# Optimization experiments

Hardware: AMD Instinct MI355X
Metric: run time of the kernel (lower is better)

Reference implementation:

```python
import jax, jax.numpy as jnp
import numpy as np

BN_EPS = 1e-5


def setup_inputs() -> dict:
    key = jax.random.key(0)
    ks = jax.random.split(key, 9)
    N, C, T, V, S, INTER, OUT = 64, 64, 300, 25, 3, 16, 64
    return {
        "x": jax.random.normal(ks[0], (N, C, T, V), dtype=jnp.float32),
        "A": jax.random.uniform(ks[1], (S, V, V), dtype=jnp.float32),
        "PA": jax.random.normal(ks[2], (S, V, V), dtype=jnp.float32) * 1e-3,
        "Wa": jax.random.normal(ks[3], (S, INTER, C), dtype=jnp.float32) * 0.1,
        "ba": jax.random.normal(ks[4], (S, INTER), dtype=jnp.float32) * 0.1,
        "Wb": jax.random.normal(ks[5], (S, INTER, C), dtype=jnp.float32) * 0.1,
        "bb": jax.random.normal(ks[6], (S, INTER), dtype=jnp.float32) * 0.1,
        "Wd": jax.random.normal(ks[7], (S, OUT, C), dtype=jnp.float32) * 0.1,
        "bd": jax.random.normal(ks[8], (S, OUT), dtype=jnp.float32) * 0.1,
        "gamma": jnp.ones((OUT,), dtype=jnp.float32),
        "beta": jnp.zeros((OUT,), dtype=jnp.float32),
    }


def reference(x, A, PA, Wa, ba, Wb, bb, Wd, bd, gamma, beta):
    N, C, T, V = x.shape
    S, INTER = Wa.shape[0], Wa.shape[1]
    K = INTER * T  # contraction length for attention

    # 1x1 convs for all subsets at once: [N,S,inter,T,V]
    fa = jnp.einsum('nctv,sic->nsitv', x, Wa) + ba[None, :, :, None, None]
    fb = jnp.einsum('nctv,sic->nsitv', x, Wb) + bb[None, :, :, None, None]

    # A1: permute(0,3,1,2).view(N,V,inter*T)  -> [N,S,V,K]
    A1 = fa.transpose(0, 1, 4, 2, 3).reshape(N, S, V, K)
    # A2: view(N,inter*T,V)                   -> [N,S,K,V]
    A2 = fb.reshape(N, S, K, V)

    # attention: softmax over dim=-2, plus learned adjacency
    att = jnp.einsum('nsvk,nskw->nsvw', A1, A2) / jnp.asarray(K, x.dtype)
    att = jax.nn.softmax(att, axis=-2) + (A + PA)[None]  # [N,S,V,V]

    # message passing: x.view(N,C*T,V) @ att, then 1x1 conv_d, summed over subsets
    xm = jnp.einsum('nkv,nsvw->nskw', x.reshape(N, C * T, V), att)
    xm = xm.reshape(N, S, C, T, V)
    y = jnp.einsum('nsctv,soc->notv', xm, Wd) + bd.sum(0)[None, :, None, None]

    # BatchNorm2d (training-mode batch stats, per-channel over N,T,V)
    mean = y.mean(axis=(0, 2, 3), keepdims=True)
    var = y.var(axis=(0, 2, 3), keepdims=True)
    y = gamma[None, :, None, None] * (y - mean) * jax.lax.rsqrt(var + BN_EPS) \
        + beta[None, :, None, None]

    # residual (in_channels == out_channels -> identity down) + relu
    return jax.nn.relu(y + x)
```

## Files before the change

### kernel.cpp

```cpp
#include <hip/hip_runtime.h>
#include <math.h>

constexpr int Nn = 64, Cc = 64, Tt = 300, Vv = 25, Ss = 3, Ii = 16, Oo = 64;
constexpr int TVc  = Tt * Vv;
constexpr int CTVc = Cc * TVc;
constexpr float KINV = 1.0f / 4800.0f;

constexpr int WS_ATT  = 0;
constexpr int WS_SUM  = 120000;
constexpr int WS_SQ   = 120512;
constexpr int WS_MEAN = 121024;
constexpr int WS_RSTD = 121088;
constexpr int WS_ZERO_FLOATS = 121024;
constexpr int WS_XB_F   = 121152;
constexpr int WS_WAB_F  = WS_XB_F + 15360000;
constexpr int WS_WDB_F  = WS_WAB_F + 3072;
constexpr int WS_ATTB_F = WS_WDB_F + 6144;
constexpr int WS_END_F  = WS_ATTB_F + 98304;
constexpr size_t WS_NEED = (size_t)WS_END_F * 4;

typedef __attribute__((ext_vector_type(8))) short bf16x8;
typedef __attribute__((ext_vector_type(4))) short short4v;
typedef __attribute__((ext_vector_type(4))) float f32x4;
typedef __attribute__((ext_vector_type(16))) float f32x16;
typedef __attribute__((ext_vector_type(4))) int int4v;

__device__ __forceinline__ short f2bf(float f) {
    unsigned u = __builtin_bit_cast(unsigned, f);
    u += 0x7FFFu + ((u >> 16) & 1u);
    return (short)(u >> 16);
}
__device__ __forceinline__ float bf2f(short s) {
    unsigned u = ((unsigned)(unsigned short)s) << 16;
    return __builtin_bit_cast(float, u);
}
__device__ __forceinline__ void store4(float* p, f32x4 v) {
    __builtin_memcpy(p, &v, 16);
}

__global__ __launch_bounds__(256) void k0_xpose(
    const float* __restrict__ x, short* __restrict__ xb)
{
    const int n   = blockIdx.y;
    const int tid = threadIdx.x;
    const int tv  = blockIdx.x * 32 + (tid & 31);
    const int g   = (tid >> 5) & 7;
    if (tv >= TVc) return;
    const float* xp = x + (size_t)n * CTVc + (size_t)(g * 8) * TVc + tv;
    bf16x8 o;
    #pragma unroll
    for (int j = 0; j < 8; ++j) o[j] = f2bf(xp[(size_t)j * TVc]);
    *(bf16x8*)(xb + ((size_t)n * TVc + tv) * 64 + g * 8) = o;
}

__global__ __launch_bounds__(256) void kpack(
    const float* __restrict__ Wa, const float* __restrict__ Wb,
    const float* __restrict__ Wd, short* __restrict__ wab, short* __restrict__ wdb)
{
    const int i = blockIdx.x * 256 + threadIdx.x;
    if (i < 6144) {
        const int s = i >> 11, rb = i & 2047, r = rb >> 6, c = rb & 63;
        const float v = (r < 16) ? Wa[(s * 16 + r) * 64 + c]
                                 : Wb[(s * 16 + (r - 16)) * 64 + c];
        wab[i] = f2bf(v);
    }
    if (i < 12288) wdb[i] = f2bf(Wd[i]);
}

template<bool XB>
__device__ __forceinline__ void load_xfrag(
    const float* __restrict__ xn, const short* __restrict__ xbn,
    int tv, bool ok, int quad, bf16x8& b0, bf16x8& b1)
{
    if constexpr (XB) {
        const short* bp = xbn + (ok ? tv : 0) * 64 + quad * 8;
        b0 = *(const bf16x8*)bp;
        b1 = *(const bf16x8*)(bp + 32);
    } else {
        const float* bp = xn + (quad * 8) * TVc + tv;
        #pragma unroll
        for (int j = 0; j < 8; ++j) {
            b0[j] = f2bf(ok ? bp[j * TVc] : 0.0f);
            b1[j] = f2bf(ok ? bp[(j + 32) * TVc] : 0.0f);
        }
    }
}

template<bool XB>
__global__ __launch_bounds__(256) void ka_gram_mfma(
    const float* __restrict__ x, const short* __restrict__ xb,
    const short* __restrict__ wab,
    const float* __restrict__ Wa, const float* __restrict__ ba,
    const float* __restrict__ Wb, const float* __restrict__ bb,
    float* __restrict__ att)
{
    __shared__ short uT[112 * 104];
    __shared__ float part[4 * 1024];
    __shared__ float bab[96];

    const int tid = threadIdx.x;
    const int t0  = blockIdx.x * 4;
    const int n   = blockIdx.y;
    const float* xn  = x + n * CTVc + t0 * 25;
    const short* xbn = XB ? (xb + ((size_t)n * TVc + t0 * 25) * 64) : nullptr;

    if (tid < 96) {
        const int s = tid >> 5, r = tid & 31;
        bab[tid] = (r < 16) ? ba[s * 16 + r] : bb[s * 16 + r - 16];
    }

    const int lane = tid & 63;
    const int wave = tid >> 6;
    const int l16  = lane & 15;
    const int quad = lane >> 4;

    bf16x8 afr[3][2][2];
    #pragma unroll
    for (int s = 0; s < 3; ++s)
        #pragma unroll
        for (int half = 0; half < 2; ++half)
            #pragma unroll
            for (int k = 0; k < 2; ++k) {
                if constexpr (XB) {
                    afr[s][half][k] = *(const bf16x8*)(
                        wab + (s * 32 + half * 16 + l16) * 64 + k * 32 + quad * 8);
                } else {
                    const float* W = half ? Wb : Wa;
                    const float* wp = W + (s * 16 + l16) * 64 + k * 32 + quad * 8;
                    const float4 w0 = *(const float4*)wp;
                    const float4 w1 = *(const float4*)(wp + 4);
                    bf16x8 a;
                    a[0] = f2bf(w0.x); a[1] = f2bf(w0.y); a[2] = f2bf(w0.z); a[3] = f2bf(w0.w);
                    a[4] = f2bf(w1.x); a[5] = f2bf(w1.y); a[6] = f2bf(w1.z); a[7] = f2bf(w1.w);
                    afr[s][half][k] = a;
                }
            }
    __syncthreads();

    for (int nt = wave; nt < 7; nt += 4) {
        const int tv = nt * 16 + l16;
        const bool ok = tv < 100;
        bf16x8 b0, b1;
        load_xfrag<XB>(xn, xbn, tv, ok, quad, b0, b1);
        #pragma unroll
        for (int s = 0; s < 3; ++s)
            #pragma unroll
            for (int half = 0; half < 2; ++half) {
                f32x4 acc = {0.0f, 0.0f, 0.0f, 0.0f};
                acc = __builtin_amdgcn_mfma_f32_16x16x32_bf16(afr[s][half][0], b0, acc, 0, 0, 0);
                acc = __builtin_amdgcn_mfma_f32_16x16x32_bf16(afr[s][half][1], b1, acc, 0, 0, 0);
                const float4 bv = *(const float4*)(bab + s * 32 + half * 16 + quad * 4);
                short4v pk;
                pk[0] = f2bf(acc[0] + bv.x); pk[1] = f2bf(acc[1] + bv.y);
                pk[2] = f2bf(acc[2] + bv.z); pk[3] = f2bf(acc[3] + bv.w);
                *(short4v*)(uT + tv * 104 + s * 32 + half * 16 + quad * 4) = pk;
            }
    }
    __syncthreads();

    const int t   = wave;
    const int w32 = lane & 31;
    const int khi = lane >> 5;
    f32x16 g[3];
    #pragma unroll
    for (int s = 0; s < 3; ++s)
        #pragma unroll
        for (int r = 0; r < 16; ++r) g[s][r] = 0.0f;

    #pragma unroll
    for (int s = 0; s < 3; ++s) {
        const short* base = uT + (t * 25 + w32) * 104 + s * 32 + khi * 8;
        const bf16x8 aA = *(const bf16x8*)(base);
        const bf16x8 bB = *(const bf16x8*)(base + 16);
        g[s] = __builtin_amdgcn_mfma_f32_32x32x16_bf16(aA, bB, g[s], 0, 0, 0);
    }

    for (int s = 0; s < 3; ++s) {
        __syncthreads();
        #pragma unroll
        for (int r = 0; r < 16; ++r) {
            const int row = (r & 3) + 8 * (r >> 2) + 4 * khi;
            part[wave * 1024 + row * 32 + w32] = g[s][r];
        }
        __syncthreads();
        float* attns = att + (n * 3 + s) * 625;
        for (int p = tid; p < 625; p += 256) {
            const int v = p / 25, w = p - v * 25;
            const int q = v * 32 + w;
            atomicAdd(attns + p, part[q] + part[1024 + q] + part[2048 + q] + part[3072 + q]);
        }
    }
}

template<bool ATTB>
__global__ __launch_bounds__(64) void kb_softmax(
    float* __restrict__ att, const float* __restrict__ A, const float* __restrict__ PA,
    short* __restrict__ attb)
{
    const int b = blockIdx.x;
    const int s = b % 3;
    const int w = threadIdx.x;
    if (w >= 32) return;
    float col[25] = {};
    if (w < 25) {
        float* base = att + b * 625;
        float m = -1e30f;
        #pragma unroll
        for (int v = 0; v < 25; ++v) {
            col[v] = base[v * 25 + w] * KINV;
            m = fmaxf(m, col[v]);
        }
        float sum = 0.0f;
        #pragma unroll
        for (int v = 0; v < 25; ++v) { col[v] = expf(col[v] - m); sum += col[v]; }
        const float inv = 1.0f / sum;
        #pragma unroll
        for (int v = 0; v < 25; ++v) {
            col[v] = fmaf(col[v], inv, A[(s * 25 + v) * 25 + w] + PA[(s * 25 + v) * 25 + w]);
            base[v * 25 + w] = col[v];
        }
    }
    if constexpr (ATTB) {
        short* dst = attb + b * 1024 + w * 32;
        #pragma unroll
        for (int v = 0; v < 25; ++v) dst[v] = (w < 25) ? f2bf(col[v]) : (short)0;
        #pragma unroll
        for (int v = 25; v < 32; ++v) dst[v] = 0;
    }
}

__global__ __launch_bounds__(512, 4) void k3_y_mfma(
    const short* __restrict__ xb, const short* __restrict__ wdb,
    const short* __restrict__ attb, float* __restrict__ y, float* __restrict__ bns)
{
    __shared__ __align__(16) short U[192 * 128];
    __shared__ float bnA[8][32], bnB[8][32];

    const int tid = threadIdx.x;
    const int t0  = blockIdx.x * 4;
    const int n   = blockIdx.y;
    const short* xbn = xb + ((size_t)n * TVc + t0 * 25) * 64;

    const int lane = tid & 63;
    const int wave = tid >> 6;
    const int l16  = lane & 15;
    const int quad = lane >> 4;

    for (int i = tid; i < 3072; i += 512)
        ((int4v*)U)[i] = (int4v){0, 0, 0, 0};
    __syncthreads();

    if (wave < 7) {
        const int tv = wave * 16 + l16;
        const bool ok = tv < 100;
        const short* bp = xbn + (ok ? tv : 0) * 64 + quad * 8;
        const bf16x8 b0 = *(const bf16x8*)bp;
        const bf16x8 b1 = *(const bf16x8*)(bp + 32);
        const int tl  = tv / 25;
        const int vp  = tv - tl * 25;
        const int col = tl * 32 + vp;
        const int grp = col >> 3, ing = col & 7;
        #pragma unroll
        for (int s = 0; s < 3; ++s)
            #pragma unroll
            for (int m = 0; m < 4; ++m) {
                const short* wp = wdb + (s * 64 + m * 16 + l16) * 64 + quad * 8;
                const bf16x8 f0 = *(const bf16x8*)wp;
                const bf16x8 f1 = *(const bf16x8*)(wp + 32);
                f32x4 acc = {0.0f, 0.0f, 0.0f, 0.0f};
                acc = __builtin_amdgcn_mfma_f32_16x16x32_bf16(f0, b0, acc, 0, 0, 0);
                acc = __builtin_amdgcn_mfma_f32_16x16x32_bf16(f1, b1, acc, 0, 0, 0);
                if (ok) {
                    #pragma unroll
                    for (int r = 0; r < 4; ++r) {
                        const int row = s * 64 + m * 16 + quad * 4 + r;
                        U[row * 128 + (((grp ^ (row & 15)) << 3) | ing)] = f2bf(acc[r]);
                    }
                }
            }
    }
    __syncthreads();

    const int t  = wave >> 1;
    const int ob = (wave & 1) * 32;
    f32x4 D[2][2];
    #pragma unroll
    for (int mt = 0; mt < 2; ++mt)
        #pragma unroll
        for (int nb = 0; nb < 2; ++nb) D[mt][nb] = (f32x4){0.0f, 0.0f, 0.0f, 0.0f};
    #pragma unroll
    for (int s = 0; s < 3; ++s) {
        const short* ab = attb + (size_t)(n * 3 + s) * 1024 + l16 * 32 + quad * 8;
        const bf16x8 a0 = *(const bf16x8*)ab;
        const bf16x8 a1 = *(const bf16x8*)(ab + 512);
        #pragma unroll
        for (int nb = 0; nb < 2; ++nb) {
            const int row = s * 64 + ob + nb * 16 + l16;
            const bf16x8 bv = *(const bf16x8*)(
                U + row * 128 + (((t * 4 + quad) ^ (row & 15)) << 3));
            D[0][nb] = __builtin_amdgcn_mfma_f32_16x16x32_bf16(a0, bv, D[0][nb], 0, 0, 0);
            D[1][nb] = __builtin_amdgcn_mfma_f32_16x16x32_bf16(a1, bv, D[1][nb], 0, 0, 0);
        }
    }

    float s1[2] = {0.0f, 0.0f}, s2[2] = {0.0f, 0.0f};
    #pragma unroll
    for (int nb = 0; nb < 2; ++nb) {
        const int og = ob + nb * 16 + l16;
        float* dst = y + ((size_t)(n * 64 + og) * 300 + t0 + t) * 25;
        const f32x4 d0 = D[0][nb];
        store4(dst + quad * 4, d0);
        s1[nb] += d0[0] + d0[1] + d0[2] + d0[3];
        s2[nb] += d0[0]*d0[0] + d0[1]*d0[1] + d0[2]*d0[2] + d0[3]*d0[3];
        const f32x4 d1 = D[1][nb];
        if (quad < 2) {
            store4(dst + 16 + quad * 4, d1);
            s1[nb] += d1[0] + d1[1] + d1[2] + d1[3];
            s2[nb] += d1[0]*d1[0] + d1[1]*d1[1] + d1[2]*d1[2] + d1[3]*d1[3];
        } else if (quad == 2) {
            dst[24] = d1[0];
            s1[nb] += d1[0];
            s2[nb] += d1[0] * d1[0];
        }
    }
    #pragma unroll
    for (int nb = 0; nb < 2; ++nb) {
        s1[nb] += __shfl_xor(s1[nb], 16); s1[nb] += __shfl_xor(s1[nb], 32);
        s2[nb] += __shfl_xor(s2[nb], 16); s2[nb] += __shfl_xor(s2[nb], 32);
    }
    if (lane < 16) {
        bnA[wave][lane]      = s1[0];
        bnA[wave][16 + lane] = s1[1];
        bnB[wave][lane]      = s2[0];
        bnB[wave][16 + lane] = s2[1];
    }
    __syncthreads();
    if (tid < 64) {
        const int o = tid, h = o >> 5, i = o & 31;
        const float S1 = bnA[h][i] + bnA[h + 2][i] + bnA[h + 4][i] + bnA[h + 6][i];
        const float S2 = bnB[h][i] + bnB[h + 2][i] + bnB[h + 4][i] + bnB[h + 6][i];
        const int cp = (blockIdx.x & 7) * 64;
        atomicAdd(bns + cp + o, S1);
        atomicAdd(bns + 512 + cp + o, S2);
    }
}

__global__ __launch_bounds__(256) void k3_y_mfma_fb(
    const float* __restrict__ x, const float* __restrict__ Wd,
    const float* __restrict__ att, float* __restrict__ y, float* __restrict__ bns)
{
    __shared__ __align__(16) short U[96 * 128];
    __shared__ __align__(16) short attT[3 * 1024];
    __shared__ float bn1[4][32], bn2[4][32];

    const int tid = threadIdx.x;
    const int t0  = blockIdx.x * 4;
    const int n   = blockIdx.y;
    const int oh  = blockIdx.z;
    const float* xn = x + n * CTVc + t0 * 25;

    const int lane = tid & 63;
    const int wave = tid >> 6;
    const int l16  = lane & 15;
    const int quad = lane >> 4;

    for (int i = tid; i < 1536; i += 256)
        ((int4v*)U)[i] = (int4v){0, 0, 0, 0};
    for (int i = tid; i < 3072; i += 256) {
        const int s = i >> 10, r = i & 1023, v = r >> 5, vp = r & 31;
        const float val = (v < 25 && vp < 25) ? att[(n * 3 + s) * 625 + vp * 25 + v] : 0.0f;
        attT[i] = f2bf(val);
    }
    bf16x8 afr[3][2][2];
    #pragma unroll
    for (int s = 0; s < 3; ++s)
        #pragma unroll
        for (int m = 0; m < 2; ++m)
            #pragma unroll
            for (int k = 0; k < 2; ++k) {
                const float* wp = Wd + ((s * 64 + oh * 32 + m * 16 + l16) * 64) + k * 32 + quad * 8;
                const float4 w0 = *(const float4*)wp;
                const float4 w1 = *(const float4*)(wp + 4);
                bf16x8 a;
                a[0] = f2bf(w0.x); a[1] = f2bf(w0.y); a[2] = f2bf(w0.z); a[3] = f2bf(w0.w);
                a[4] = f2bf(w1.x); a[5] = f2bf(w1.y); a[6] = f2bf(w1.z); a[7] = f2bf(w1.w);
                afr[s][m][k] = a;
            }
    __syncthreads();

    for (int nt = wave; nt < 7; nt += 4) {
        const int tv = nt * 16 + l16;
        const bool ok = tv < 100;
        bf16x8 b0, b1;
        load_xfrag<false>(xn, nullptr, tv, ok, quad, b0, b1);
        const int tl  = tv / 25;
        const int vp  = tv - tl * 25;
        const int col = tl * 32 + vp;
        const int grp = col >> 3, ing = col & 7;
        #pragma unroll
        for (int s = 0; s < 3; ++s)
            #pragma unroll
            for (int m = 0; m < 2; ++m) {
                f32x4 acc = {0.0f, 0.0f, 0.0f, 0.0f};
                acc = __builtin_amdgcn_mfma_f32_16x16x32_bf16(afr[s][m][0], b0, acc, 0, 0, 0);
                acc = __builtin_amdgcn_mfma_f32_16x16x32_bf16(afr[s][m][1], b1, acc, 0, 0, 0);
                if (ok) {
                    #pragma unroll
                    for (int r = 0; r < 4; ++r) {
                        const int row = s * 32 + m * 16 + quad * 4 + r;
                        U[row * 128 + (((grp ^ (row & 15)) << 3) | ing)] = f2bf(acc[r]);
                    }
                }
            }
    }
    __syncthreads();

    const int t = wave;
    bf16x8 aF[3][2], bF[3][2];
    #pragma unroll
    for (int s = 0; s < 3; ++s) {
        #pragma unroll
        for (int mt = 0; mt < 2; ++mt)
            aF[s][mt] = *(const bf16x8*)(attT + s * 1024 + (mt * 16 + l16) * 32 + quad * 8);
        #pragma unroll
        for (int nb = 0; nb < 2; ++nb) {
            const int row = s * 32 + nb * 16 + l16;
            bF[s][nb] = *(const bf16x8*)(U + row * 128 + (((t * 4 + quad) ^ (row & 15)) << 3));
        }
    }
    f32x4 D[2][2];
    #pragma unroll
    for (int mt = 0; mt < 2; ++mt)
        #pragma unroll
        for (int nb = 0; nb < 2; ++nb) D[mt][nb] = (f32x4){0.0f, 0.0f, 0.0f, 0.0f};
    #pragma unroll
    for (int s = 0; s < 3; ++s)
        #pragma unroll
        for (int mt = 0; mt < 2; ++mt)
            #pragma unroll
            for (int nb = 0; nb < 2; ++nb)
                D[mt][nb] = __builtin_amdgcn_mfma_f32_16x16x32_bf16(aF[s][mt], bF[s][nb], D[mt][nb], 0, 0, 0);

    float s1[2] = {0.0f, 0.0f}, s2[2] = {0.0f, 0.0f};
    #pragma unroll
    for (int nb = 0; nb < 2; ++nb) {
        const int og = oh * 32 + nb * 16 + l16;
        float* dst = y + ((size_t)(n * 64 + og) * 300 + t0 + t) * 25;
        const f32x4 d0 = D[0][nb];
        store4(dst + quad * 4, d0);
        s1[nb] += d0[0] + d0[1] + d0[2] + d0[3];
        s2[nb] += d0[0]*d0[0] + d0[1]*d0[1] + d0[2]*d0[2] + d0[3]*d0[3];
        const f32x4 d1 = D[1][nb];
        if (quad < 2) {
            store4(dst + 16 + quad * 4, d1);
            s1[nb] += d1[0] + d1[1] + d1[2] + d1[3];
            s2[nb] += d1[0]*d1[0] + d1[1]*d1[1] + d1[2]*d1[2] + d1[3]*d1[3];
        } else if (quad == 2) {
            dst[24] = d1[0];
            s1[nb] += d1[0];
            s2[nb] += d1[0] * d1[0];
        }
    }
    #pragma unroll
    for (int nb = 0; nb < 2; ++nb) {
        s1[nb] += __shfl_xor(s1[nb], 16); s1[nb] += __shfl_xor(s1[nb], 32);
        s2[nb] += __shfl_xor(s2[nb], 16); s2[nb] += __shfl_xor(s2[nb], 32);
    }
    if (lane < 16) {
        bn1[wave][lane]      = s1[0];
        bn1[wave][16 + lane] = s1[1];
        bn2[wave][lane]      = s2[0];
        bn2[wave][16 + lane] = s2[1];
    }
    __syncthreads();
    if (tid < 32) {
        const float S1 = bn1[0][tid] + bn1[1][tid] + bn1[2][tid] + bn1[3][tid];
        const float S2 = bn2[0][tid] + bn2[1][tid] + bn2[2][tid] + bn2[3][tid];
        const int cp = (blockIdx.x & 7) * 64;
        atomicAdd(bns + cp + oh * 32 + tid, S1);
        atomicAdd(bns + 512 + cp + oh * 32 + tid, S2);
    }
}

__global__ __launch_bounds__(64) void k3b_stats(float* __restrict__ ws)
{
    const int o = threadIdx.x;
    if (o >= 64) return;
    const float cnt_inv = 1.0f / 480000.0f;
    float s = 0.0f, q = 0.0f;
    #pragma unroll
    for (int j = 0; j < 8; ++j) {
        s += ws[WS_SUM + j * 64 + o];
        q += ws[WS_SQ  + j * 64 + o];
    }
    const float mean = s * cnt_inv;
    const float var  = q * cnt_inv - mean * mean;
    ws[WS_MEAN + o] = mean;
    ws[WS_RSTD + o] = rsqrtf(var + 1e-5f);
}

__global__ __launch_bounds__(256) void k4_bn(
    float* __restrict__ out, const float* __restrict__ x,
    const float* __restrict__ gamma, const float* __restrict__ beta,
    const float* __restrict__ ws)
{
    const int o = blockIdx.y, n = blockIdx.z;
    const int j = blockIdx.x * 256 + threadIdx.x;
    if (j >= 1875) return;
    const size_t i4 = (size_t)(n * 64 + o) * 1875 + j;
    const float mean = ws[WS_MEAN + o], rstd = ws[WS_RSTD + o];
    const float g = gamma[o], b = beta[o];
    const float4 yv = ((const float4*)out)[i4];
    const float4 xv = ((const float4*)x)[i4];
    float4 r;
    r.x = fmaxf(fmaf(g * (yv.x - mean), rstd, b) + xv.x, 0.0f);
    r.y = fmaxf(fmaf(g * (yv.y - mean), rstd, b) + xv.y, 0.0f);
    r.z = fmaxf(fmaf(g * (yv.z - mean), rstd, b) + xv.z, 0.0f);
    r.w = fmaxf(fmaf(g * (yv.w - mean), rstd, b) + xv.w, 0.0f);
    ((float4*)out)[i4] = r;
}

extern "C" void kernel_launch(void* const* d_in, const int* in_sizes, int n_in,
                              void* d_out, int out_size, void* d_ws, size_t ws_size,
                              hipStream_t stream)
{
    const float* x  = (const float*)d_in[0];
    const float* A  = (const float*)d_in[1];
    const float* PA = (const float*)d_in[2];
    const float* Wa = (const float*)d_in[3];
    const float* ba = (const float*)d_in[4];
    const float* Wb = (const float*)d_in[5];
    const float* bb = (const float*)d_in[6];
    const float* Wd = (const float*)d_in[7];
    const float* gamma = (const float*)d_in[9];
    const float* beta  = (const float*)d_in[10];
    float* out = (float*)d_out;
    float* ws  = (float*)d_ws;

    hipMemsetAsync(d_ws, 0, (size_t)WS_ZERO_FLOATS * sizeof(float), stream);

    if (ws_size >= WS_NEED) {
        short* xbp  = (short*)(ws + WS_XB_F);
        short* wab  = (short*)(ws + WS_WAB_F);
        short* wdb  = (short*)(ws + WS_WDB_F);
        short* attb = (short*)(ws + WS_ATTB_F);
        k0_xpose<<<dim3(235, 64), 256, 0, stream>>>(x, xbp);
        kpack<<<dim3(48), 256, 0, stream>>>(Wa, Wb, Wd, wab, wdb);
        ka_gram_mfma<true><<<dim3(75, 64), 256, 0, stream>>>(
            x, xbp, wab, Wa, ba, Wb, bb, ws + WS_ATT);
        kb_softmax<true><<<dim3(192), 64, 0, stream>>>(ws + WS_ATT, A, PA, attb);
        k3_y_mfma<<<dim3(75, 64), 512, 0, stream>>>(xbp, wdb, attb, out, ws + WS_SUM);
    } else {
        ka_gram_mfma<false><<<dim3(75, 64), 256, 0, stream>>>(
            x, nullptr, nullptr, Wa, ba, Wb, bb, ws + WS_ATT);
        kb_softmax<false><<<dim3(192), 64, 0, stream>>>(ws + WS_ATT, A, PA, nullptr);
        k3_y_mfma_fb<<<dim3(75, 64, 2), 256, 0, stream>>>(
            x, Wd, ws + WS_ATT, out, ws + WS_SUM);
    }
    k3b_stats<<<dim3(1), 64, 0, stream>>>(ws);
    k4_bn<<<dim3(8, 64, 64), 256, 0, stream>>>(out, x, gamma, beta, ws);
}
```

Measured before the change: 484.7 us.

## Process three time tiles per k3 block with prefetched x loads

The k3_y_mfma kernel now loops over three 4-timestep tiles per block instead of one, cutting the grid from 75 to 25 blocks per sample. It hoists the attention fragment loads out of the loop and prefetches the next tile's x fragments while the current tile is computed. BN partial sums accumulate in registers across tiles before the atomics. This amortizes block setup, the U zeroing, attention loads and atomics, but adds an extra barrier per tile, fewer blocks for occupancy, and a raised launch-bounds occupancy target that may pressure registers.

```diff
diff --git a/kernel.cpp b/kernel.cpp
--- a/kernel.cpp
+++ b/kernel.cpp
@@ -229,7 +229,9 @@
     }
 }
 
-__global__ __launch_bounds__(512, 4) void k3_y_mfma(
+constexpr int K3_TILES = 3;
+
+__global__ __launch_bounds__(512, 6) void k3_y_mfma(
     const short* __restrict__ xb, const short* __restrict__ wdb,
     const short* __restrict__ attb, float* __restrict__ y, float* __restrict__ bns)
 {
@@ -237,9 +239,8 @@
     __shared__ float bnA[8][32], bnB[8][32];
 
     const int tid = threadIdx.x;
-    const int t0  = blockIdx.x * 4;
     const int n   = blockIdx.y;
-    const short* xbn = xb + ((size_t)n * TVc + t0 * 25) * 64;
+    const int tb0 = blockIdx.x * K3_TILES;
 
     const int lane = tid & 63;
     const int wave = tid >> 6;
@@ -248,81 +249,106 @@
 
     for (int i = tid; i < 3072; i += 512)
         ((int4v*)U)[i] = (int4v){0, 0, 0, 0};
-    __syncthreads();
-
-    if (wave < 7) {
-        const int tv = wave * 16 + l16;
-        const bool ok = tv < 100;
-        const short* bp = xbn + (ok ? tv : 0) * 64 + quad * 8;
-        const bf16x8 b0 = *(const bf16x8*)bp;
-        const bf16x8 b1 = *(const bf16x8*)(bp + 32);
-        const int tl  = tv / 25;
-        const int vp  = tv - tl * 25;
-        const int col = tl * 32 + vp;
-        const int grp = col >> 3, ing = col & 7;
-        #pragma unroll
-        for (int s = 0; s < 3; ++s)
-            #pragma unroll
-            for (int m = 0; m < 4; ++m) {
-                const short* wp = wdb + (s * 64 + m * 16 + l16) * 64 + quad * 8;
-                const bf16x8 f0 = *(const bf16x8*)wp;
-                const bf16x8 f1 = *(const bf16x8*)(wp + 32);
-                f32x4 acc = {0.0f, 0.0f, 0.0f, 0.0f};
-                acc = __builtin_amdgcn_mfma_f32_16x16x32_bf16(f0, b0, acc, 0, 0, 0);
-                acc = __builtin_amdgcn_mfma_f32_16x16x32_bf16(f1, b1, acc, 0, 0, 0);
-                if (ok) {
-                    #pragma unroll
-                    for (int r = 0; r < 4; ++r) {
-                        const int row = s * 64 + m * 16 + quad * 4 + r;
-                        U[row * 128 + (((grp ^ (row & 15)) << 3) | ing)] = f2bf(acc[r]);
+
+    bf16x8 a0[3], a1[3];
+    #pragma unroll
+    for (int s = 0; s < 3; ++s) {
+        const short* ab = attb + (size_t)(n * 3 + s) * 1024 + l16 * 32 + quad * 8;
+        a0[s] = *(const bf16x8*)ab;
+        a1[s] = *(const bf16x8*)(ab + 512);
+    }
+
+    const int tv  = (wave < 7) ? wave * 16 + l16 : 0;
+    const bool ok = (wave < 7) && (tv < 100);
+    const int tl  = tv / 25;
+    const int vp  = tv - tl * 25;
+    const int col = tl * 32 + vp;
+    const int grp = col >> 3, ing = col & 7;
+
+    const short* xtile = xb + ((size_t)n * TVc + tb0 * 100) * 64;
+    const int xoff = (ok ? tv : 0) * 64 + quad * 8;
+
+    bf16x8 bc0 = *(const bf16x8*)(xtile + xoff);
+    bf16x8 bc1 = *(const bf16x8*)(xtile + xoff + 32);
+    bf16x8 nx0, nx1;
+
+    const int t  = wave >> 1;
+    const int ob = (wave & 1) * 32;
+    float s1[2] = {0.0f, 0.0f}, s2[2] = {0.0f, 0.0f};
+
+    __syncthreads();
+
+    #pragma unroll
+    for (int it = 0; it < K3_TILES; ++it) {
+        if (it + 1 < K3_TILES) {
+            const short* bp = xtile + (it + 1) * 6400 + xoff;
+            nx0 = *(const bf16x8*)bp;
+            nx1 = *(const bf16x8*)(bp + 32);
+        }
+
+        if (wave < 7) {
+            #pragma unroll
+            for (int s = 0; s < 3; ++s)
+                #pragma unroll
+                for (int m = 0; m < 4; ++m) {
+                    const short* wp = wdb + (s * 64 + m * 16 + l16) * 64 + quad * 8;
+                    const bf16x8 f0 = *(const bf16x8*)wp;
+                    const bf16x8 f1 = *(const bf16x8*)(wp + 32);
+                    f32x4 acc = {0.0f, 0.0f, 0.0f, 0.0f};
+                    acc = __builtin_amdgcn_mfma_f32_16x16x32_bf16(f0, bc0, acc, 0, 0, 0);
+                    acc = __builtin_amdgcn_mfma_f32_16x16x32_bf16(f1, bc1, acc, 0, 0, 0);
+                    if (ok) {
+                        #pragma unroll
+                        for (int r = 0; r < 4; ++r) {
+                            const int row = s * 64 + m * 16 + quad * 4 + r;
+                            U[row * 128 + (((grp ^ (row & 15)) << 3) | ing)] = f2bf(acc[r]);
+                        }
                     }
                 }
+        }
+        __syncthreads();
+
+        f32x4 D[2][2];
+        #pragma unroll
+        for (int mt = 0; mt < 2; ++mt)
+            #pragma unroll
+            for (int nb = 0; nb < 2; ++nb) D[mt][nb] = (f32x4){0.0f, 0.0f, 0.0f, 0.0f};
+        #pragma unroll
+        for (int s = 0; s < 3; ++s) {
+            #pragma unroll
+            for (int nb = 0; nb < 2; ++nb) {
+                const int row = s * 64 + ob + nb * 16 + l16;
+                const bf16x8 bv = *(const bf16x8*)(
+                    U + row * 128 + (((t * 4 + quad) ^ (row & 15)) << 3));
+                D[0][nb] = __builtin_amdgcn_mfma_f32_16x16x32_bf16(a0[s], bv, D[0][nb], 0, 0, 0);
+                D[1][nb] = __builtin_amdgcn_mfma_f32_16x16x32_bf16(a1[s], bv, D[1][nb], 0, 0, 0);
             }
-    }
-    __syncthreads();
-
-    const int t  = wave >> 1;
-    const int ob = (wave & 1) * 32;
-    f32x4 D[2][2];
-    #pragma unroll
-    for (int mt = 0; mt < 2; ++mt)
-        #pragma unroll
-        for (int nb = 0; nb < 2; ++nb) D[mt][nb] = (f32x4){0.0f, 0.0f, 0.0f, 0.0f};
-    #pragma unroll
-    for (int s = 0; s < 3; ++s) {
-        const short* ab = attb + (size_t)(n * 3 + s) * 1024 + l16 * 32 + quad * 8;
-        const bf16x8 a0 = *(const bf16x8*)ab;
-        const bf16x8 a1 = *(const bf16x8*)(ab + 512);
+        }
+
+        const int t0 = (tb0 + it) * 4;
         #pragma unroll
         for (int nb = 0; nb < 2; ++nb) {
-            const int row = s * 64 + ob + nb * 16 + l16;
-            const bf16x8 bv = *(const bf16x8*)(
-                U + row * 128 + (((t * 4 + quad) ^ (row & 15)) << 3));
-            D[0][nb] = __builtin_amdgcn_mfma_f32_16x16x32_bf16(a0, bv, D[0][nb], 0, 0, 0);
-            D[1][nb] = __builtin_amdgcn_mfma_f32_16x16x32_bf16(a1, bv, D[1][nb], 0, 0, 0);
-        }
-    }
-
-    float s1[2] = {0.0f, 0.0f}, s2[2] = {0.0f, 0.0f};
-    #pragma unroll
-    for (int nb = 0; nb < 2; ++nb) {
-        const int og = ob + nb * 16 + l16;
-        float* dst = y + ((size_t)(n * 64 + og) * 300 + t0 + t) * 25;
-        const f32x4 d0 = D[0][nb];
-        store4(dst + quad * 4, d0);
-        s1[nb] += d0[0] + d0[1] + d0[2] + d0[3];
-        s2[nb] += d0[0]*d0[0] + d0[1]*d0[1] + d0[2]*d0[2] + d0[3]*d0[3];
-        const f32x4 d1 = D[1][nb];
-        if (quad < 2) {
-            store4(dst + 16 + quad * 4, d1);
-            s1[nb] += d1[0] + d1[1] + d1[2] + d1[3];
-            s2[nb] += d1[0]*d1[0] + d1[1]*d1[1] + d1[2]*d1[2] + d1[3]*d1[3];
-        } else if (quad == 2) {
-            dst[24] = d1[0];
-            s1[nb] += d1[0];
-            s2[nb] += d1[0] * d1[0];
-        }
-    }
+            const int og = ob + nb * 16 + l16;
+            float* dst = y + ((size_t)(n * 64 + og) * 300 + t0 + t) * 25;
+            const f32x4 d0 = D[0][nb];
+            store4(dst + quad * 4, d0);
+            s1[nb] += d0[0] + d0[1] + d0[2] + d0[3];
+            s2[nb] += d0[0]*d0[0] + d0[1]*d0[1] + d0[2]*d0[2] + d0[3]*d0[3];
+            const f32x4 d1 = D[1][nb];
+            if (quad < 2) {
+                store4(dst + 16 + quad * 4, d1);
+                s1[nb] += d1[0] + d1[1] + d1[2] + d1[3];
+                s2[nb] += d1[0]*d1[0] + d1[1]*d1[1] + d1[2]*d1[2] + d1[3]*d1[3];
+            } else if (quad == 2) {
+                dst[24] = d1[0];
+                s1[nb] += d1[0];
+                s2[nb] += d1[0] * d1[0];
+            }
+        }
+        __syncthreads();
+        if (it + 1 < K3_TILES) { bc0 = nx0; bc1 = nx1; }
+    }
+
     #pragma unroll
     for (int nb = 0; nb < 2; ++nb) {
         s1[nb] += __shfl_xor(s1[nb], 16); s1[nb] += __shfl_xor(s1[nb], 32);
@@ -549,7 +575,7 @@
         ka_gram_mfma<true><<<dim3(75, 64), 256, 0, stream>>>(
             x, xbp, wab, Wa, ba, Wb, bb, ws + WS_ATT);
         kb_softmax<true><<<dim3(192), 64, 0, stream>>>(ws + WS_ATT, A, PA, attb);
-        k3_y_mfma<<<dim3(75, 64), 512, 0, stream>>>(xbp, wdb, attb, out, ws + WS_SUM);
+        k3_y_mfma<<<dim3(25, 64), 512, 0, stream>>>(xbp, wdb, attb, out, ws + WS_SUM);
     } else {
         ka_gram_mfma<false><<<dim3(75, 64), 256, 0, stream>>>(
             x, nullptr, nullptr, Wa, ba, Wb, bb, ws + WS_ATT);
```

After: 499.6 us. 1.03x slower.
